# Performance work log

Measured on AMD Instinct MI355X. Metric: run time of the kernel, lower is better.

Reference implementation:

```python
import jax, jax.numpy as jnp
import numpy as np

D = 768
HID = 4 * D
B = 16
HRES = 32
WRES = 32
T = HRES * WRES


def layernorm(x, g, b, eps=1e-5):
    m = jnp.mean(x, axis=-1, keepdims=True)
    v = jnp.mean(jnp.square(x - m), axis=-1, keepdims=True)
    return (x - m) * jax.lax.rsqrt(v + eps) * g + b


def q_shift(x, H, W):
    # Vision-RWKV quad-directional token shift: split channels into 4 groups,
    # each group takes the neighboring patch's value in one direction (zero pad).
    Bn, N, C = x.shape
    xi = x.reshape(Bn, H, W, C)
    c = C // 4
    g0 = jnp.pad(xi[:, :, :-1, 0 * c:1 * c], ((0, 0), (0, 0), (1, 0), (0, 0)))  # from left
    g1 = jnp.pad(xi[:, :, 1:, 1 * c:2 * c], ((0, 0), (0, 0), (0, 1), (0, 0)))   # from right
    g2 = jnp.pad(xi[:, :-1, :, 2 * c:3 * c], ((0, 0), (1, 0), (0, 0), (0, 0)))  # from above
    g3 = jnp.pad(xi[:, 1:, :, 3 * c:4 * c], ((0, 0), (0, 1), (0, 0), (0, 0)))   # from below
    return jnp.concatenate([g0, g1, g2, g3], axis=-1).reshape(Bn, N, C)


def wkv_scan(w_log, u, k, v):
    # Numerically stable RWKV WKV recurrence (per-channel linear attention).
    # k, v: [B, T, C]; w = -exp(w_log) is the per-channel decay, u the bonus.
    w = -jnp.exp(w_log)
    kT = jnp.swapaxes(k, 0, 1)  # [T, B, C]
    vT = jnp.swapaxes(v, 0, 1)
    Bn, C = k.shape[0], k.shape[2]
    aa0 = jnp.zeros((Bn, C), k.dtype)
    bb0 = jnp.zeros((Bn, C), k.dtype)
    pp0 = jnp.full((Bn, C), -1e30, k.dtype)

    def step(carry, kv):
        aa, bb, pp = carry
        kt, vt = kv
        ww = u + kt
        p = jnp.maximum(pp, ww)
        e1 = jnp.exp(pp - p)
        e2 = jnp.exp(ww - p)
        out = (e1 * aa + e2 * vt) / (e1 * bb + e2)
        ww2 = pp + w
        p2 = jnp.maximum(ww2, kt)
        e1b = jnp.exp(ww2 - p2)
        e2b = jnp.exp(kt - p2)
        return (e1b * aa + e2b * vt, e1b * bb + e2b, p2), out

    _, outT = jax.lax.scan(step, (aa0, bb0, pp0), (kT, vT))
    return jnp.swapaxes(outT, 0, 1)  # [B, T, C]


def setup_inputs() -> dict:
    key = jax.random.key(0)
    ks = jax.random.split(key, 16)

    def nrm(k, shape, s=0.02):
        return jax.random.normal(k, shape, jnp.float32) * s

    return {
        "x": jax.random.normal(ks[0], (B, T, D), jnp.float32),
        "H": HRES,
        "W": WRES,
        "ln1_g": jnp.ones((D,), jnp.float32),
        "ln1_b": jnp.zeros((D,), jnp.float32),
        "ln2_g": jnp.ones((D,), jnp.float32),
        "ln2_b": jnp.zeros((D,), jnp.float32),
        "mu_k": jax.random.uniform(ks[1], (D,), jnp.float32),
        "mu_v": jax.random.uniform(ks[2], (D,), jnp.float32),
        "mu_r": jax.random.uniform(ks[3], (D,), jnp.float32),
        "w_log": nrm(ks[4], (D,), 0.5),
        "u": nrm(ks[5], (D,), 0.5),
        "Wk": nrm(ks[6], (D, D)),
        "Wv": nrm(ks[7], (D, D)),
        "Wr": nrm(ks[8], (D, D)),
        "Wo": nrm(ks[9], (D, D)),
        "cmu_k": jax.random.uniform(ks[10], (D,), jnp.float32),
        "cmu_r": jax.random.uniform(ks[11], (D,), jnp.float32),
        "Ck": nrm(ks[12], (HID, D)),
        "Cv": nrm(ks[13], (D, HID)),
        "Cr": nrm(ks[14], (D, D)),
    }


def reference(x, H, W, ln1_g, ln1_b, ln2_g, ln2_b, mu_k, mu_v, mu_r, w_log, u,
              Wk, Wv, Wr, Wo, cmu_k, cmu_r, Ck, Cv, Cr):
    h = x
    # ---- spatial mix (RWKV time-mix over patch sequence) ----
    a = layernorm(h, ln1_g, ln1_b)
    sx = q_shift(a, H, W)
    xk = a * mu_k + sx * (1.0 - mu_k)
    xv = a * mu_v + sx * (1.0 - mu_v)
    xr = a * mu_r + sx * (1.0 - mu_r)
    k = xk @ Wk.T
    v = xv @ Wv.T
    r = jax.nn.sigmoid(xr @ Wr.T)
    wkv = wkv_scan(w_log, u, k, v)
    h = h + (r * wkv) @ Wo.T
    # ---- channel mix (squared-ReLU gated FFN) ----
    a2 = layernorm(h, ln2_g, ln2_b)
    sx2 = q_shift(a2, H, W)
    xk2 = a2 * cmu_k + sx2 * (1.0 - cmu_k)
    xr2 = a2 * cmu_r + sx2 * (1.0 - cmu_r)
    kk = jnp.square(jax.nn.relu(xk2 @ Ck.T))
    h = h + jax.nn.sigmoid(xr2 @ Cr.T) * (kk @ Cv.T)
    # ---- outer residual from RWKVBlock.forward ----
    return h + x
```

## Files before the change

kernel.cpp:

```cpp
#include <hip/hip_runtime.h>
#include <hip/hip_bf16.h>

#define DD   768
#define TT   1024
#define BBATCH 16
#define NROWS (BBATCH * TT)
#define HIDN 3072
#define HHALF 1536
#define HH 32
#define WW 32
#define DW  (DD * DD)
#define DH  (DD * HIDN)
#define CCH 64
#define PCH (TT / CCH)

typedef float  floatx4 __attribute__((ext_vector_type(4)));
typedef __bf16 bf16x8  __attribute__((ext_vector_type(8)));

__device__ __forceinline__ float bf2f(__hip_bfloat16 v) { return __bfloat162float(v); }
__device__ __forceinline__ __hip_bfloat16 f2bf(float v) { return __float2bfloat16(v); }
__device__ __forceinline__ float toF(__hip_bfloat16 v) { return __bfloat162float(v); }
__device__ __forceinline__ float toF(float v) { return v; }

#define GL2LDS(gp, lp)  __builtin_amdgcn_global_load_lds(                     \
    (const __attribute__((address_space(1))) void*)(gp),                      \
    (__attribute__((address_space(3))) void*)(lp), 16, 0, 0)

__global__ __launch_bounds__(256)
void cvt_all(const float* __restrict__ w0, const float* __restrict__ w1,
             const float* __restrict__ w2, const float* __restrict__ w3,
             const float* __restrict__ w4, const float* __restrict__ w5,
             const float* __restrict__ w6, __hip_bfloat16* __restrict__ dst)
{
    const int b = blockIdx.x;
    const float* s; size_t dofs; int rel;
    if (b < 2880) {
        const int seg = b / 576; rel = b - seg * 576;
        s = seg == 0 ? w0 : seg == 1 ? w1 : seg == 2 ? w2 : seg == 3 ? w3 : w4;
        dofs = (size_t)seg * DW;
    } else if (b < 5184) {
        rel = b - 2880; s = w5; dofs = 5ull * DW;
    } else {
        rel = b - 5184; s = w6; dofs = 5ull * DW + DH;
    }
    const int i = rel * 1024 + threadIdx.x * 4;
    const float4 v = *reinterpret_cast<const float4*>(s + i);
    __hip_bfloat16 o[4] = {f2bf(v.x), f2bf(v.y), f2bf(v.z), f2bf(v.w)};
    *reinterpret_cast<ushort4*>(&dst[dofs + i]) = *reinterpret_cast<const ushort4*>(o);
}

template <typename TIN>
__global__ __launch_bounds__(256)
void ln_stats_k(const TIN* __restrict__ x,
                float* __restrict__ mean, float* __restrict__ rstd)
{
    const int row = blockIdx.x, tid = threadIdx.x;
    const int lane = tid & 63, wid = tid >> 6;
    const TIN* xr = x + (size_t)row * DD;
    float s1 = 0.f, s2 = 0.f;
#pragma unroll
    for (int i = 0; i < 3; ++i) {
        const float v = toF(xr[tid + i * 256]);
        s1 += v; s2 += v * v;
    }
#pragma unroll
    for (int off = 32; off > 0; off >>= 1) {
        s1 += __shfl_down(s1, off);
        s2 += __shfl_down(s2, off);
    }
    __shared__ float sh[8];
    if (lane == 0) { sh[wid] = s1; sh[4 + wid] = s2; }
    __syncthreads();
    if (tid == 0) {
        s1 = sh[0] + sh[1] + sh[2] + sh[3];
        s2 = sh[4] + sh[5] + sh[6] + sh[7];
        const float m = s1 * (1.f / DD);
        mean[row] = m;
        rstd[row] = rsqrtf(s2 * (1.f / DD) - m * m + 1e-5f);
    }
}

template <typename TIN>
__device__ __forceinline__ float ln_at(const TIN* __restrict__ x,
                                       const float* __restrict__ mean,
                                       const float* __restrict__ rstd,
                                       const float* __restrict__ g,
                                       const float* __restrict__ b,
                                       int grow, int c)
{
    return (toF(x[(size_t)grow * DD + c]) - mean[grow]) * rstd[grow] * g[c] + b[c];
}

template <typename TIN, int NOUT>
__global__ __launch_bounds__(256)
void mix_k(const TIN* __restrict__ x,
           const float* __restrict__ mean, const float* __restrict__ rstd,
           const float* __restrict__ g, const float* __restrict__ b,
           const float* __restrict__ muk,
           const float* __restrict__ muv,
           const float* __restrict__ mur,
           __hip_bfloat16* __restrict__ xk,
           __hip_bfloat16* __restrict__ xv,
           __hip_bfloat16* __restrict__ xr)
{
    const size_t idx = (size_t)blockIdx.x * 256 + threadIdx.x;
    const int c  = (int)(idx % DD);
    const int n  = (int)((idx / DD) % TT);
    const int bb = (int)(idx / ((size_t)DD * TT));
    const int y = n >> 5, xp = n & 31;
    const int grow = bb * TT + n;

    const float av = ln_at(x, mean, rstd, g, b, grow, c);

    const int grp = c / (DD / 4);
    int ny = y, nx = xp; bool ok;
    if      (grp == 0) { nx = xp - 1; ok = xp > 0;      }
    else if (grp == 1) { nx = xp + 1; ok = xp < WW - 1; }
    else if (grp == 2) { ny = y - 1;  ok = y > 0;       }
    else               { ny = y + 1;  ok = y < HH - 1;  }
    const float sx = ok ? ln_at(x, mean, rstd, g, b, bb * TT + ny * WW + nx, c) : 0.f;

    const float mk = muk[c], mr = mur[c];
    xk[idx] = f2bf(av * mk + sx * (1.f - mk));
    xr[idx] = f2bf(av * mr + sx * (1.f - mr));
    if (NOUT == 3) {
        const float mv = muv[c];
        xv[idx] = f2bf(av * mv + sx * (1.f - mv));
    }
}

#define BM 128
#define BN 128
#define BKK 64

__device__ __forceinline__ void gemm_core(
    const __hip_bfloat16* __restrict__ A, const __hip_bfloat16* __restrict__ W,
    int K, int Wstr, int bm, int bn, unsigned short* lds, floatx4 acc[4][4])
{
    const int tid  = threadIdx.x;
    const int lane = tid & 63, wid = tid >> 6;
    const int l15  = lane & 15, quad = lane >> 4;
    const int m0   = (wid & 1) * 64;
    const int n0   = (wid >> 1) * 64;
    const int srow  = lane >> 3;
    const int gcolg = (lane & 7) ^ srow;
    const int s0    = wid * 4;
    const int swzbase = l15 & 7;

    for (int k0 = 0; k0 < K; k0 += BKK) {
#pragma unroll
        for (int t = 0; t < 4; ++t) {
            const int s   = s0 + t;
            const int row = s * 8 + srow;
            GL2LDS(A + (size_t)(bm * BM + row) * K    + k0 + gcolg * 8,
                   &lds[s * 512]);
            GL2LDS(W + (size_t)(bn * BN + row) * Wstr + k0 + gcolg * 8,
                   &lds[8192 + s * 512]);
        }
        __syncthreads();
#pragma unroll
        for (int kk = 0; kk < BKK; kk += 32) {
            const int swz = (((kk >> 3) + quad) ^ swzbase) * 8;
            bf16x8 af[4], bfr[4];
#pragma unroll
            for (int i = 0; i < 4; ++i)
                af[i] = *reinterpret_cast<const bf16x8*>(
                    &lds[(m0 + i * 16 + l15) * BKK + swz]);
#pragma unroll
            for (int j = 0; j < 4; ++j)
                bfr[j] = *reinterpret_cast<const bf16x8*>(
                    &lds[8192 + (n0 + j * 16 + l15) * BKK + swz]);
#pragma unroll
            for (int i = 0; i < 4; ++i)
#pragma unroll
                for (int j = 0; j < 4; ++j)
                    acc[i][j] = __builtin_amdgcn_mfma_f32_16x16x32_bf16(
                        af[i], bfr[j], acc[i][j], 0, 0, 0);
        }
        __syncthreads();
    }
}

__device__ __forceinline__ void xpose_band(const floatx4 accRow[4], float* scr,
                                           int lane, float cv[16])
{
    const int l15 = lane & 15, quad = lane >> 4;
#pragma unroll
    for (int j = 0; j < 4; ++j)
#pragma unroll
        for (int r = 0; r < 4; ++r)
            scr[(quad * 4 + r) * 68 + j * 16 + l15] = accRow[j][r];
    const int row_l = lane >> 2, cb = (lane & 3) * 16;
#pragma unroll
    for (int q = 0; q < 4; ++q)
        *reinterpret_cast<float4*>(&cv[q * 4]) =
            *reinterpret_cast<const float4*>(&scr[row_l * 68 + cb + q * 4]);
}

template <int MODE>
__global__ __launch_bounds__(256, 2)
void gemm_bt(const __hip_bfloat16* __restrict__ A,
             const __hip_bfloat16* __restrict__ W,
             int K, int Wstr, int Nn,
             __hip_bfloat16* __restrict__ outB,
             float* __restrict__ outF,
             const __hip_bfloat16* __restrict__ auxS,
             const __hip_bfloat16* __restrict__ auxH,
             const float* __restrict__ auxX)
{
    __shared__ __align__(16) unsigned short lds[16384];
    const int bm = blockIdx.x, bn = blockIdx.y;
    const int tid = threadIdx.x, lane = tid & 63, wid = tid >> 6;
    const int m0 = (wid & 1) * 64, n0 = (wid >> 1) * 64;

    floatx4 acc[4][4];
#pragma unroll
    for (int i = 0; i < 4; ++i)
#pragma unroll
        for (int j = 0; j < 4; ++j)
            acc[i][j] = floatx4{0.f, 0.f, 0.f, 0.f};

    gemm_core(A, W, K, Wstr, bm, bn, lds, acc);

    float* scr = reinterpret_cast<float*>(lds) + wid * 1088;
    const int row_l = lane >> 2, cb = (lane & 3) * 16;
#pragma unroll
    for (int i = 0; i < 4; ++i) {
        float cv[16];
        xpose_band(acc[i], scr, lane, cv);
        const int grow = bm * BM + m0 + i * 16 + row_l;
        const int gcol = bn * BN + n0 + cb;
        const size_t idx = (size_t)grow * Nn + gcol;
        if (MODE == 1 || MODE == 3) {
            __hip_bfloat16 ob[16];
#pragma unroll
            for (int e = 0; e < 16; ++e) {
                float v = cv[e];
                if (MODE == 1) v = 1.f / (1.f + __expf(-v));
                else { v = fmaxf(v, 0.f); v = v * v; }
                ob[e] = f2bf(v);
            }
            *reinterpret_cast<uint4*>(&outB[idx])     = *reinterpret_cast<const uint4*>(&ob[0]);
            *reinterpret_cast<uint4*>(&outB[idx + 8]) = *reinterpret_cast<const uint4*>(&ob[8]);
        } else if (MODE == 2) {
            float xv[16];
#pragma unroll
            for (int q = 0; q < 4; ++q)
                *reinterpret_cast<float4*>(&xv[q * 4]) =
                    *reinterpret_cast<const float4*>(&auxX[idx + q * 4]);
            __hip_bfloat16 ob[16];
#pragma unroll
            for (int e = 0; e < 16; ++e) ob[e] = f2bf(cv[e] + xv[e]);
            *reinterpret_cast<uint4*>(&outB[idx])     = *reinterpret_cast<const uint4*>(&ob[0]);
            *reinterpret_cast<uint4*>(&outB[idx + 8]) = *reinterpret_cast<const uint4*>(&ob[8]);
        } else if (MODE == 4) {
            unsigned short hs[16], ss[16]; float xv[16], ov[16];
            *reinterpret_cast<uint4*>(&hs[0]) = *reinterpret_cast<const uint4*>(&auxH[idx]);
            *reinterpret_cast<uint4*>(&hs[8]) = *reinterpret_cast<const uint4*>(&auxH[idx + 8]);
            *reinterpret_cast<uint4*>(&ss[0]) = *reinterpret_cast<const uint4*>(&auxS[idx]);
            *reinterpret_cast<uint4*>(&ss[8]) = *reinterpret_cast<const uint4*>(&auxS[idx + 8]);
#pragma unroll
            for (int q = 0; q < 4; ++q)
                *reinterpret_cast<float4*>(&xv[q * 4]) =
                    *reinterpret_cast<const float4*>(&auxX[idx + q * 4]);
#pragma unroll
            for (int e = 0; e < 16; ++e)
                ov[e] = bf2f(__hip_bfloat16_raw{hs[e]})
                      + bf2f(__hip_bfloat16_raw{ss[e]}) * cv[e] + xv[e];
#pragma unroll
            for (int q = 0; q < 4; ++q)
                *reinterpret_cast<float4*>(&outF[idx + q * 4]) =
                    *reinterpret_cast<const float4*>(&ov[q * 4]);
        } else {
            unsigned short ss[16]; float ov[16];
            *reinterpret_cast<uint4*>(&ss[0]) = *reinterpret_cast<const uint4*>(&auxS[idx]);
            *reinterpret_cast<uint4*>(&ss[8]) = *reinterpret_cast<const uint4*>(&auxS[idx + 8]);
#pragma unroll
            for (int q = 0; q < 4; ++q)
                *reinterpret_cast<float4*>(&ov[q * 4]) =
                    *reinterpret_cast<const float4*>(&outF[idx + q * 4]);
#pragma unroll
            for (int e = 0; e < 16; ++e)
                ov[e] += bf2f(__hip_bfloat16_raw{ss[e]}) * cv[e];
#pragma unroll
            for (int q = 0; q < 4; ++q)
                *reinterpret_cast<float4*>(&outF[idx + q * 4]) =
                    *reinterpret_cast<const float4*>(&ov[q * 4]);
        }
    }
}

__global__ __launch_bounds__(256, 2)
void gemm_qkv(const __hip_bfloat16* __restrict__ A0, const __hip_bfloat16* __restrict__ A1,
              const __hip_bfloat16* __restrict__ A2,
              const __hip_bfloat16* __restrict__ W0, const __hip_bfloat16* __restrict__ W1,
              const __hip_bfloat16* __restrict__ W2,
              __hip_bfloat16* __restrict__ O0, __hip_bfloat16* __restrict__ O1,
              __hip_bfloat16* __restrict__ O2)
{
    __shared__ __align__(16) unsigned short lds[16384];
    const int z = blockIdx.z;
    const __hip_bfloat16* A = z == 0 ? A0 : z == 1 ? A1 : A2;
    const __hip_bfloat16* W = z == 0 ? W0 : z == 1 ? W1 : W2;
    __hip_bfloat16*       O = z == 0 ? O0 : z == 1 ? O1 : O2;
    const int bm = blockIdx.x, bn = blockIdx.y;
    const int tid = threadIdx.x, lane = tid & 63, wid = tid >> 6;
    const int m0 = (wid & 1) * 64, n0 = (wid >> 1) * 64;

    floatx4 acc[4][4];
#pragma unroll
    for (int i = 0; i < 4; ++i)
#pragma unroll
        for (int j = 0; j < 4; ++j)
            acc[i][j] = floatx4{0.f, 0.f, 0.f, 0.f};

    gemm_core(A, W, DD, DD, bm, bn, lds, acc);

    float* scr = reinterpret_cast<float*>(lds) + wid * 1088;
    const int row_l = lane >> 2, cb = (lane & 3) * 16;
#pragma unroll
    for (int i = 0; i < 4; ++i) {
        float cv[16];
        xpose_band(acc[i], scr, lane, cv);
        const int grow = bm * BM + m0 + i * 16 + row_l;
        const int gcol = bn * BN + n0 + cb;
        const size_t idx = (size_t)grow * DD + gcol;
        __hip_bfloat16 ob[16];
#pragma unroll
        for (int e = 0; e < 16; ++e) {
            float v = cv[e];
            if (z == 2) v = 1.f / (1.f + __expf(-v));
            ob[e] = f2bf(v);
        }
        *reinterpret_cast<uint4*>(&O[idx])     = *reinterpret_cast<const uint4*>(&ob[0]);
        *reinterpret_cast<uint4*>(&O[idx + 8]) = *reinterpret_cast<const uint4*>(&ob[8]);
    }
}

__global__ __launch_bounds__(256)
void wkv_passA(const float* __restrict__ w_log,
               const __hip_bfloat16* __restrict__ k,
               const __hip_bfloat16* __restrict__ v,
               float* __restrict__ SA, float* __restrict__ SB,
               float* __restrict__ SP)
{
    const int c  = blockIdx.x * 256 + threadIdx.x;
    const int j  = blockIdx.y;
    const int bb = blockIdx.z;
    const float w = -__expf(w_log[c]);
    const size_t base = ((size_t)bb * TT + j * CCH) * DD + c;
    float a = 0.f, b = 0.f, p = -1e30f;
#pragma unroll 4
    for (int t = 0; t < CCH; ++t) {
        const size_t o = base + (size_t)t * DD;
        const float kt = bf2f(k[o]);
        const float vt = bf2f(v[o]);
        const float ww2 = p + w;
        const float p2  = fmaxf(ww2, kt);
        const float e1  = __expf(ww2 - p2);
        const float e2  = __expf(kt - p2);
        a = e1 * a + e2 * vt;
        b = e1 * b + e2;
        p = p2;
    }
    const size_t si = ((size_t)bb * PCH + j) * DD + c;
    SA[si] = a; SB[si] = b; SP[si] = p;
}

__global__ __launch_bounds__(256)
void wkv_scanj(const float* __restrict__ w_log,
               float* __restrict__ SA, float* __restrict__ SB,
               float* __restrict__ SP)
{
    const int idx = blockIdx.x * 256 + threadIdx.x;
    const int c = idx % DD, bb = idx / DD;
    const float wC = -__expf(w_log[c]) * (float)CCH;
    float a = 0.f, b = 0.f, p = -1e30f;
#pragma unroll
    for (int j = 0; j < PCH; ++j) {
        const size_t si = ((size_t)bb * PCH + j) * DD + c;
        const float aj = SA[si], bj = SB[si], pj = SP[si];
        SA[si] = a; SB[si] = b; SP[si] = p;
        const float pd = p + wC;
        const float pn = fmaxf(pd, pj);
        const float e1 = __expf(pd - pn);
        const float e2 = __expf(pj - pn);
        a = e1 * a + e2 * aj;
        b = e1 * b + e2 * bj;
        p = pn;
    }
}

__global__ __launch_bounds__(256)
void wkv_passB(const float* __restrict__ w_log, const float* __restrict__ u,
               const __hip_bfloat16* __restrict__ k,
               const __hip_bfloat16* __restrict__ v,
               const __hip_bfloat16* __restrict__ r,
               __hip_bfloat16* __restrict__ rw,
               const float* __restrict__ SA, const float* __restrict__ SB,
               const float* __restrict__ SP)
{
    const int c  = blockIdx.x * 256 + threadIdx.x;
    const int j  = blockIdx.y;
    const int bb = blockIdx.z;
    const float w  = -__expf(w_log[c]);
    const float uu = u[c];
    const size_t si = ((size_t)bb * PCH + j) * DD + c;
    float aa = SA[si], bbv = SB[si], pp = SP[si];
    const size_t base = ((size_t)bb * TT + j * CCH) * DD + c;
#pragma unroll 4
    for (int t = 0; t < CCH; ++t) {
        const size_t o = base + (size_t)t * DD;
        const float kt = bf2f(k[o]);
        const float vt = bf2f(v[o]);
        const float rt = bf2f(r[o]);
        const float ww = uu + kt;
        const float p  = fmaxf(pp, ww);
        const float e1 = __expf(pp - p);
        const float e2 = __expf(ww - p);
        const float ov = __fdividef(e1 * aa + e2 * vt, e1 * bbv + e2);
        rw[o] = f2bf(rt * ov);
        const float ww2 = pp + w;
        const float p2  = fmaxf(ww2, kt);
        const float e1b = __expf(ww2 - p2);
        const float e2b = __expf(kt - p2);
        aa  = e1b * aa + e2b * vt;
        bbv = e1b * bbv + e2b;
        pp  = p2;
    }
}

extern "C" void kernel_launch(void* const* d_in, const int* in_sizes, int n_in,
                              void* d_out, int out_size, void* d_ws, size_t ws_size,
                              hipStream_t stream)
{
    (void)in_sizes; (void)n_in; (void)out_size;
    const float* x     = (const float*)d_in[0];
    const float* ln1_g = (const float*)d_in[3];
    const float* ln1_b = (const float*)d_in[4];
    const float* ln2_g = (const float*)d_in[5];
    const float* ln2_b = (const float*)d_in[6];
    const float* mu_k  = (const float*)d_in[7];
    const float* mu_v  = (const float*)d_in[8];
    const float* mu_r  = (const float*)d_in[9];
    const float* w_log = (const float*)d_in[10];
    const float* u     = (const float*)d_in[11];
    const float* Wk    = (const float*)d_in[12];
    const float* Wv    = (const float*)d_in[13];
    const float* Wr    = (const float*)d_in[14];
    const float* Wo    = (const float*)d_in[15];
    const float* cmu_k = (const float*)d_in[16];
    const float* cmu_r = (const float*)d_in[17];
    const float* Ck    = (const float*)d_in[18];
    const float* Cv    = (const float*)d_in[19];
    const float* Cr    = (const float*)d_in[20];
    float* out = (float*)d_out;

    const size_t ND = (size_t)NROWS * DD;
    const size_t SL = ND * 2;
    const size_t WBYTES = (size_t)(5 * DW + 2 * DH) * 2;
    const size_t NSTATE = (size_t)BBATCH * PCH * DD;
    const size_t NEED = 5 * SL + WBYTES
                      + 2 * (size_t)NROWS * sizeof(float)
                      + 3 * NSTATE * sizeof(float);
    if (ws_size < NEED) return;

    char* w = (char*)d_ws;
    __hip_bfloat16* S0 = (__hip_bfloat16*)(w);
    __hip_bfloat16* S1 = (__hip_bfloat16*)(w + 1 * SL);
    __hip_bfloat16* S2 = (__hip_bfloat16*)(w + 2 * SL);
    __hip_bfloat16* S3 = (__hip_bfloat16*)(w + 3 * SL);
    __hip_bfloat16* S4 = (__hip_bfloat16*)(w + 4 * SL);
    __hip_bfloat16* WB  = (__hip_bfloat16*)(w + 5 * SL);
    __hip_bfloat16* WkB = WB;
    __hip_bfloat16* WvB = WB + 1ull * DW;
    __hip_bfloat16* WrB = WB + 2ull * DW;
    __hip_bfloat16* WoB = WB + 3ull * DW;
    __hip_bfloat16* CrB = WB + 4ull * DW;
    __hip_bfloat16* CkB = WB + 5ull * DW;
    __hip_bfloat16* CvB = CkB + DH;
    float* meanB = (float*)(w + 5 * SL + WBYTES);
    float* rstdB = meanB + NROWS;
    float* SAb = rstdB + NROWS;
    float* SBb = SAb + NSTATE;
    float* SPb = SBb + NSTATE;

    const int EW_GRID = (int)(ND / 256);
    const dim3 g768(NROWS / BM, DD / BN);
    const dim3 g1536(NROWS / BM, HHALF / BN);
    const dim3 gqkv(NROWS / BM, DD / BN, 3);
    const dim3 gwkv(DD / 256, PCH, BBATCH);

    cvt_all<<<7488, 256, 0, stream>>>(Wk, Wv, Wr, Wo, Cr, Ck, Cv, WB);

    ln_stats_k<float><<<NROWS, 256, 0, stream>>>(x, meanB, rstdB);
    mix_k<float, 3><<<EW_GRID, 256, 0, stream>>>(x, meanB, rstdB, ln1_g, ln1_b,
                                                 mu_k, mu_v, mu_r, S0, S1, S2);
    gemm_qkv<<<dim3(NROWS / BM, DD / BN, 2), 256, 0, stream>>>(
        S0, S1, nullptr, WkB, WvB, nullptr, S3, S4, nullptr);
    gemm_bt<1><<<g768, 256, 0, stream>>>(S2, WrB, DD, DD, DD, S0, nullptr,
                                         nullptr, nullptr, nullptr);
    wkv_passA<<<gwkv, 256, 0, stream>>>(w_log, S3, S4, SAb, SBb, SPb);
    wkv_scanj<<<(BBATCH * DD) / 256, 256, 0, stream>>>(w_log, SAb, SBb, SPb);
    wkv_passB<<<gwkv, 256, 0, stream>>>(w_log, u, S3, S4, S0, S1, SAb, SBb, SPb);
    gemm_bt<2><<<g768, 256, 0, stream>>>(S1, WoB, DD, DD, DD, S2, nullptr,
                                         nullptr, nullptr, x);

    ln_stats_k<__hip_bfloat16><<<NROWS, 256, 0, stream>>>(S2, meanB, rstdB);
    mix_k<__hip_bfloat16, 2><<<EW_GRID, 256, 0, stream>>>(S2, meanB, rstdB, ln2_g, ln2_b,
                                                          cmu_k, nullptr, cmu_r, S0, nullptr, S3);
    gemm_bt<1><<<g768, 256, 0, stream>>>(S3, CrB, DD, DD, DD, S1, nullptr,
                                         nullptr, nullptr, nullptr);
    __hip_bfloat16* kk = S3;
    gemm_bt<3><<<g1536, 256, 0, stream>>>(S0, CkB, DD, DD, HHALF,
                                          kk, nullptr, nullptr, nullptr, nullptr);
    gemm_bt<4><<<g768, 256, 0, stream>>>(kk, CvB, HHALF, HIDN, DD,
                                         nullptr, out, S1, S2, x);
    gemm_bt<3><<<g1536, 256, 0, stream>>>(S0, CkB + (size_t)HHALF * DD, DD, DD, HHALF,
                                          kk, nullptr, nullptr, nullptr, nullptr);
    gemm_bt<5><<<g768, 256, 0, stream>>>(kk, CvB + HHALF, HHALF, HIDN, DD,
                                         nullptr, out, S1, nullptr, nullptr);
}
```

Before: 566.7 us.

## Vectorize LN/mix kernels and use extra workspace to fuse Wr and full-width FFN GEMMs

Vectorizes the layernorm statistics and token-shift mix kernels to four elements per thread, with one wave per row instead of a block-level reduction. When the workspace is large enough, it launches the receptance projection inside the batched QKV GEMM and runs the channel-mix Ck/Cv GEMMs at full hidden width instead of two halves. A six-slot variant writes the sigmoid gate to the output buffer and reads it back in a new epilogue. The aim is fewer launches, less partial-sum traffic and better memory coalescing, at the cost of more workspace and added code paths that depend on the workspace size.

```diff
diff --git a/kernel.cpp b/kernel.cpp
--- a/kernel.cpp
+++ b/kernel.cpp
@@ -22,6 +22,18 @@
 __device__ __forceinline__ float toF(__hip_bfloat16 v) { return __bfloat162float(v); }
 __device__ __forceinline__ float toF(float v) { return v; }
 
+__device__ __forceinline__ void load4f(const float* __restrict__ p, float o[4]) {
+    const float4 v = *reinterpret_cast<const float4*>(p);
+    o[0] = v.x; o[1] = v.y; o[2] = v.z; o[3] = v.w;
+}
+__device__ __forceinline__ void load4f(const __hip_bfloat16* __restrict__ p, float o[4]) {
+    const ushort4 v = *reinterpret_cast<const ushort4*>(p);
+    o[0] = bf2f(__hip_bfloat16_raw{v.x});
+    o[1] = bf2f(__hip_bfloat16_raw{v.y});
+    o[2] = bf2f(__hip_bfloat16_raw{v.z});
+    o[3] = bf2f(__hip_bfloat16_raw{v.w});
+}
+
 #define GL2LDS(gp, lp)  __builtin_amdgcn_global_load_lds(                     \
     (const __attribute__((address_space(1))) void*)(gp),                      \
     (__attribute__((address_space(3))) void*)(lp), 16, 0, 0)
@@ -54,41 +66,27 @@
 void ln_stats_k(const TIN* __restrict__ x,
                 float* __restrict__ mean, float* __restrict__ rstd)
 {
-    const int row = blockIdx.x, tid = threadIdx.x;
-    const int lane = tid & 63, wid = tid >> 6;
+    const int row  = blockIdx.x * 4 + (threadIdx.x >> 6);
+    const int lane = threadIdx.x & 63;
     const TIN* xr = x + (size_t)row * DD;
     float s1 = 0.f, s2 = 0.f;
 #pragma unroll
-    for (int i = 0; i < 3; ++i) {
-        const float v = toF(xr[tid + i * 256]);
-        s1 += v; s2 += v * v;
+    for (int q = 0; q < 3; ++q) {
+        float v4[4];
+        load4f(xr + 4 * lane + 256 * q, v4);
+#pragma unroll
+        for (int e = 0; e < 4; ++e) { s1 += v4[e]; s2 += v4[e] * v4[e]; }
     }
 #pragma unroll
     for (int off = 32; off > 0; off >>= 1) {
         s1 += __shfl_down(s1, off);
         s2 += __shfl_down(s2, off);
     }
-    __shared__ float sh[8];
-    if (lane == 0) { sh[wid] = s1; sh[4 + wid] = s2; }
-    __syncthreads();
-    if (tid == 0) {
-        s1 = sh[0] + sh[1] + sh[2] + sh[3];
-        s2 = sh[4] + sh[5] + sh[6] + sh[7];
+    if (lane == 0) {
         const float m = s1 * (1.f / DD);
         mean[row] = m;
         rstd[row] = rsqrtf(s2 * (1.f / DD) - m * m + 1e-5f);
     }
-}
-
-template <typename TIN>
-__device__ __forceinline__ float ln_at(const TIN* __restrict__ x,
-                                       const float* __restrict__ mean,
-                                       const float* __restrict__ rstd,
-                                       const float* __restrict__ g,
-                                       const float* __restrict__ b,
-                                       int grow, int c)
-{
-    return (toF(x[(size_t)grow * DD + c]) - mean[grow]) * rstd[grow] * g[c] + b[c];
 }
 
 template <typename TIN, int NOUT>
@@ -103,14 +101,12 @@
            __hip_bfloat16* __restrict__ xv,
            __hip_bfloat16* __restrict__ xr)
 {
-    const size_t idx = (size_t)blockIdx.x * 256 + threadIdx.x;
-    const int c  = (int)(idx % DD);
-    const int n  = (int)((idx / DD) % TT);
-    const int bb = (int)(idx / ((size_t)DD * TT));
+    const size_t i4 = ((size_t)blockIdx.x * 256 + threadIdx.x) * 4;
+    const int c  = (int)(i4 % DD);
+    const int n  = (int)((i4 / DD) % TT);
+    const int bb = (int)(i4 / ((size_t)DD * TT));
     const int y = n >> 5, xp = n & 31;
     const int grow = bb * TT + n;
-
-    const float av = ln_at(x, mean, rstd, g, b, grow, c);
 
     const int grp = c / (DD / 4);
     int ny = y, nx = xp; bool ok;
@@ -118,14 +114,48 @@
     else if (grp == 1) { nx = xp + 1; ok = xp < WW - 1; }
     else if (grp == 2) { ny = y - 1;  ok = y > 0;       }
     else               { ny = y + 1;  ok = y < HH - 1;  }
-    const float sx = ok ? ln_at(x, mean, rstd, g, b, bb * TT + ny * WW + nx, c) : 0.f;
-
-    const float mk = muk[c], mr = mur[c];
-    xk[idx] = f2bf(av * mk + sx * (1.f - mk));
-    xr[idx] = f2bf(av * mr + sx * (1.f - mr));
+
+    const float4 gv = *reinterpret_cast<const float4*>(g + c);
+    const float4 bv = *reinterpret_cast<const float4*>(b + c);
+    const float gg[4] = {gv.x, gv.y, gv.z, gv.w};
+    const float bbv[4] = {bv.x, bv.y, bv.z, bv.w};
+
+    float xc[4];
+    load4f(x + (size_t)grow * DD + c, xc);
+    const float m = mean[grow], rs = rstd[grow];
+    float av[4], sx[4] = {0.f, 0.f, 0.f, 0.f};
+#pragma unroll
+    for (int e = 0; e < 4; ++e) av[e] = (xc[e] - m) * rs * gg[e] + bbv[e];
+
+    if (ok) {
+        const int nrow = bb * TT + ny * WW + nx;
+        float xn[4];
+        load4f(x + (size_t)nrow * DD + c, xn);
+        const float m2 = mean[nrow], rs2 = rstd[nrow];
+#pragma unroll
+        for (int e = 0; e < 4; ++e) sx[e] = (xn[e] - m2) * rs2 * gg[e] + bbv[e];
+    }
+
+    const float4 mkv = *reinterpret_cast<const float4*>(muk + c);
+    const float4 mrv = *reinterpret_cast<const float4*>(mur + c);
+    const float mk[4] = {mkv.x, mkv.y, mkv.z, mkv.w};
+    const float mr[4] = {mrv.x, mrv.y, mrv.z, mrv.w};
+    __hip_bfloat16 ok4[4], or4[4];
+#pragma unroll
+    for (int e = 0; e < 4; ++e) {
+        ok4[e] = f2bf(av[e] * mk[e] + sx[e] * (1.f - mk[e]));
+        or4[e] = f2bf(av[e] * mr[e] + sx[e] * (1.f - mr[e]));
+    }
+    *reinterpret_cast<ushort4*>(&xk[i4]) = *reinterpret_cast<const ushort4*>(ok4);
+    *reinterpret_cast<ushort4*>(&xr[i4]) = *reinterpret_cast<const ushort4*>(or4);
     if (NOUT == 3) {
-        const float mv = muv[c];
-        xv[idx] = f2bf(av * mv + sx * (1.f - mv));
+        const float4 mvv = *reinterpret_cast<const float4*>(muv + c);
+        const float mv[4] = {mvv.x, mvv.y, mvv.z, mvv.w};
+        __hip_bfloat16 ov4[4];
+#pragma unroll
+        for (int e = 0; e < 4; ++e)
+            ov4[e] = f2bf(av[e] * mv[e] + sx[e] * (1.f - mv[e]));
+        *reinterpret_cast<ushort4*>(&xv[i4]) = *reinterpret_cast<const ushort4*>(ov4);
     }
 }
 
@@ -206,7 +236,8 @@
              float* __restrict__ outF,
              const __hip_bfloat16* __restrict__ auxS,
              const __hip_bfloat16* __restrict__ auxH,
-             const float* __restrict__ auxX)
+             const float* __restrict__ auxX,
+             const float* __restrict__ auxG)
 {
     __shared__ __align__(16) unsigned short lds[16384];
     const int bm = blockIdx.x, bn = blockIdx.y;
@@ -271,7 +302,7 @@
             for (int q = 0; q < 4; ++q)
                 *reinterpret_cast<float4*>(&outF[idx + q * 4]) =
                     *reinterpret_cast<const float4*>(&ov[q * 4]);
-        } else {
+        } else if (MODE == 5) {
             unsigned short ss[16]; float ov[16];
             *reinterpret_cast<uint4*>(&ss[0]) = *reinterpret_cast<const uint4*>(&auxS[idx]);
             *reinterpret_cast<uint4*>(&ss[8]) = *reinterpret_cast<const uint4*>(&auxS[idx + 8]);
@@ -282,6 +313,33 @@
 #pragma unroll
             for (int e = 0; e < 16; ++e)
                 ov[e] += bf2f(__hip_bfloat16_raw{ss[e]}) * cv[e];
+#pragma unroll
+            for (int q = 0; q < 4; ++q)
+                *reinterpret_cast<float4*>(&outF[idx + q * 4]) =
+                    *reinterpret_cast<const float4*>(&ov[q * 4]);
+        } else if (MODE == 6) {
+            unsigned short hs[16]; float xv[16], gf[16], ov[16];
+            *reinterpret_cast<uint4*>(&hs[0]) = *reinterpret_cast<const uint4*>(&auxH[idx]);
+            *reinterpret_cast<uint4*>(&hs[8]) = *reinterpret_cast<const uint4*>(&auxH[idx + 8]);
+#pragma unroll
+            for (int q = 0; q < 4; ++q) {
+                *reinterpret_cast<float4*>(&xv[q * 4]) =
+                    *reinterpret_cast<const float4*>(&auxX[idx + q * 4]);
+                *reinterpret_cast<float4*>(&gf[q * 4]) =
+                    *reinterpret_cast<const float4*>(&auxG[idx + q * 4]);
+            }
+#pragma unroll
+            for (int e = 0; e < 16; ++e)
+                ov[e] = bf2f(__hip_bfloat16_raw{hs[e]}) + gf[e] * cv[e] + xv[e];
+#pragma unroll
+            for (int q = 0; q < 4; ++q)
+                *reinterpret_cast<float4*>(&outF[idx + q * 4]) =
+                    *reinterpret_cast<const float4*>(&ov[q * 4]);
+        } else {
+            float ov[16];
+#pragma unroll
+            for (int e = 0; e < 16; ++e)
+                ov[e] = 1.f / (1.f + __expf(-cv[e]));
 #pragma unroll
             for (int q = 0; q < 4; ++q)
                 *reinterpret_cast<float4*>(&outF[idx + q * 4]) =
@@ -460,10 +518,13 @@
     const size_t SL = ND * 2;
     const size_t WBYTES = (size_t)(5 * DW + 2 * DH) * 2;
     const size_t NSTATE = (size_t)BBATCH * PCH * DD;
-    const size_t NEED = 5 * SL + WBYTES
-                      + 2 * (size_t)NROWS * sizeof(float)
+    const size_t TAIL = WBYTES + 2 * (size_t)NROWS * sizeof(float)
                       + 3 * NSTATE * sizeof(float);
-    if (ws_size < NEED) return;
+    int nslots;
+    if      (ws_size >= 7 * SL + TAIL) nslots = 7;
+    else if (ws_size >= 6 * SL + TAIL) nslots = 6;
+    else if (ws_size >= 5 * SL + TAIL) nslots = 5;
+    else return;
 
     char* w = (char*)d_ws;
     __hip_bfloat16* S0 = (__hip_bfloat16*)(w);
@@ -471,7 +532,8 @@
     __hip_bfloat16* S2 = (__hip_bfloat16*)(w + 2 * SL);
     __hip_bfloat16* S3 = (__hip_bfloat16*)(w + 3 * SL);
     __hip_bfloat16* S4 = (__hip_bfloat16*)(w + 4 * SL);
-    __hip_bfloat16* WB  = (__hip_bfloat16*)(w + 5 * SL);
+    __hip_bfloat16* S5 = (__hip_bfloat16*)(w + 5 * SL);
+    __hip_bfloat16* WB  = (__hip_bfloat16*)(w + (size_t)nslots * SL);
     __hip_bfloat16* WkB = WB;
     __hip_bfloat16* WvB = WB + 1ull * DW;
     __hip_bfloat16* WrB = WB + 2ull * DW;
@@ -479,45 +541,85 @@
     __hip_bfloat16* CrB = WB + 4ull * DW;
     __hip_bfloat16* CkB = WB + 5ull * DW;
     __hip_bfloat16* CvB = CkB + DH;
-    float* meanB = (float*)(w + 5 * SL + WBYTES);
+    float* meanB = (float*)(w + (size_t)nslots * SL + WBYTES);
     float* rstdB = meanB + NROWS;
     float* SAb = rstdB + NROWS;
     float* SBb = SAb + NSTATE;
     float* SPb = SBb + NSTATE;
 
-    const int EW_GRID = (int)(ND / 256);
+    const int LN_GRID  = NROWS / 4;
+    const int MIX_GRID = (int)(ND / 1024);
     const dim3 g768(NROWS / BM, DD / BN);
     const dim3 g1536(NROWS / BM, HHALF / BN);
-    const dim3 gqkv(NROWS / BM, DD / BN, 3);
+    const dim3 gCk(NROWS / BM, HIDN / BN);
+    const dim3 gqkv3(NROWS / BM, DD / BN, 3);
+    const dim3 gqkv2(NROWS / BM, DD / BN, 2);
     const dim3 gwkv(DD / 256, PCH, BBATCH);
 
     cvt_all<<<7488, 256, 0, stream>>>(Wk, Wv, Wr, Wo, Cr, Ck, Cv, WB);
 
-    ln_stats_k<float><<<NROWS, 256, 0, stream>>>(x, meanB, rstdB);
-    mix_k<float, 3><<<EW_GRID, 256, 0, stream>>>(x, meanB, rstdB, ln1_g, ln1_b,
-                                                 mu_k, mu_v, mu_r, S0, S1, S2);
-    gemm_qkv<<<dim3(NROWS / BM, DD / BN, 2), 256, 0, stream>>>(
-        S0, S1, nullptr, WkB, WvB, nullptr, S3, S4, nullptr);
-    gemm_bt<1><<<g768, 256, 0, stream>>>(S2, WrB, DD, DD, DD, S0, nullptr,
-                                         nullptr, nullptr, nullptr);
-    wkv_passA<<<gwkv, 256, 0, stream>>>(w_log, S3, S4, SAb, SBb, SPb);
-    wkv_scanj<<<(BBATCH * DD) / 256, 256, 0, stream>>>(w_log, SAb, SBb, SPb);
-    wkv_passB<<<gwkv, 256, 0, stream>>>(w_log, u, S3, S4, S0, S1, SAb, SBb, SPb);
-    gemm_bt<2><<<g768, 256, 0, stream>>>(S1, WoB, DD, DD, DD, S2, nullptr,
-                                         nullptr, nullptr, x);
-
-    ln_stats_k<__hip_bfloat16><<<NROWS, 256, 0, stream>>>(S2, meanB, rstdB);
-    mix_k<__hip_bfloat16, 2><<<EW_GRID, 256, 0, stream>>>(S2, meanB, rstdB, ln2_g, ln2_b,
-                                                          cmu_k, nullptr, cmu_r, S0, nullptr, S3);
-    gemm_bt<1><<<g768, 256, 0, stream>>>(S3, CrB, DD, DD, DD, S1, nullptr,
-                                         nullptr, nullptr, nullptr);
-    __hip_bfloat16* kk = S3;
-    gemm_bt<3><<<g1536, 256, 0, stream>>>(S0, CkB, DD, DD, HHALF,
-                                          kk, nullptr, nullptr, nullptr, nullptr);
-    gemm_bt<4><<<g768, 256, 0, stream>>>(kk, CvB, HHALF, HIDN, DD,
-                                         nullptr, out, S1, S2, x);
-    gemm_bt<3><<<g1536, 256, 0, stream>>>(S0, CkB + (size_t)HHALF * DD, DD, DD, HHALF,
-                                          kk, nullptr, nullptr, nullptr, nullptr);
-    gemm_bt<5><<<g768, 256, 0, stream>>>(kk, CvB + HHALF, HHALF, HIDN, DD,
-                                         nullptr, out, S1, nullptr, nullptr);
-}
+    ln_stats_k<float><<<LN_GRID, 256, 0, stream>>>(x, meanB, rstdB);
+    mix_k<float, 3><<<MIX_GRID, 256, 0, stream>>>(x, meanB, rstdB, ln1_g, ln1_b,
+                                                  mu_k, mu_v, mu_r, S0, S1, S2);
+
+    if (nslots == 7) {
+        gemm_qkv<<<gqkv3, 256, 0, stream>>>(S0, S1, S2, WkB, WvB, WrB, S3, S4, S5);
+        wkv_passA<<<gwkv, 256, 0, stream>>>(w_log, S3, S4, SAb, SBb, SPb);
+        wkv_scanj<<<(BBATCH * DD) / 256, 256, 0, stream>>>(w_log, SAb, SBb, SPb);
+        wkv_passB<<<gwkv, 256, 0, stream>>>(w_log, u, S3, S4, S5, S1, SAb, SBb, SPb);
+        gemm_bt<2><<<g768, 256, 0, stream>>>(S1, WoB, DD, DD, DD, S2, nullptr,
+                                             nullptr, nullptr, x, nullptr);
+        ln_stats_k<__hip_bfloat16><<<LN_GRID, 256, 0, stream>>>(S2, meanB, rstdB);
+        mix_k<__hip_bfloat16, 2><<<MIX_GRID, 256, 0, stream>>>(S2, meanB, rstdB, ln2_g, ln2_b,
+                                                               cmu_k, nullptr, cmu_r,
+                                                               S0, nullptr, S3);
+        gemm_bt<1><<<g768, 256, 0, stream>>>(S3, CrB, DD, DD, DD, S1, nullptr,
+                                             nullptr, nullptr, nullptr, nullptr);
+        gemm_bt<3><<<gCk, 256, 0, stream>>>(S0, CkB, DD, DD, HIDN,
+                                            S3, nullptr, nullptr, nullptr, nullptr, nullptr);
+        gemm_bt<4><<<g768, 256, 0, stream>>>(S3, CvB, HIDN, HIDN, DD,
+                                             nullptr, out, S1, S2, x, nullptr);
+    } else if (nslots == 6) {
+        gemm_qkv<<<gqkv3, 256, 0, stream>>>(S0, S1, S2, WkB, WvB, WrB, S3, S4, S5);
+        wkv_passA<<<gwkv, 256, 0, stream>>>(w_log, S3, S4, SAb, SBb, SPb);
+        wkv_scanj<<<(BBATCH * DD) / 256, 256, 0, stream>>>(w_log, SAb, SBb, SPb);
+        wkv_passB<<<gwkv, 256, 0, stream>>>(w_log, u, S3, S4, S5, S0, SAb, SBb, SPb);
+        gemm_bt<2><<<g768, 256, 0, stream>>>(S0, WoB, DD, DD, DD, S1, nullptr,
+                                             nullptr, nullptr, x, nullptr);
+        ln_stats_k<__hip_bfloat16><<<LN_GRID, 256, 0, stream>>>(S1, meanB, rstdB);
+        mix_k<__hip_bfloat16, 2><<<MIX_GRID, 256, 0, stream>>>(S1, meanB, rstdB, ln2_g, ln2_b,
+                                                               cmu_k, nullptr, cmu_r,
+                                                               S0, nullptr, S2);
+        gemm_bt<7><<<g768, 256, 0, stream>>>(S2, CrB, DD, DD, DD, nullptr, out,
+                                             nullptr, nullptr, nullptr, nullptr);
+        gemm_bt<3><<<gCk, 256, 0, stream>>>(S0, CkB, DD, DD, HIDN,
+                                            S2, nullptr, nullptr, nullptr, nullptr, nullptr);
+        gemm_bt<6><<<g768, 256, 0, stream>>>(S2, CvB, HIDN, HIDN, DD,
+                                             nullptr, out, nullptr, S1, x, out);
+    } else {
+        gemm_qkv<<<gqkv2, 256, 0, stream>>>(S0, S1, nullptr, WkB, WvB, nullptr,
+                                            S3, S4, nullptr);
+        gemm_bt<1><<<g768, 256, 0, stream>>>(S2, WrB, DD, DD, DD, S0, nullptr,
+                                             nullptr, nullptr, nullptr, nullptr);
+        wkv_passA<<<gwkv, 256, 0, stream>>>(w_log, S3, S4, SAb, SBb, SPb);
+        wkv_scanj<<<(BBATCH * DD) / 256, 256, 0, stream>>>(w_log, SAb, SBb, SPb);
+        wkv_passB<<<gwkv, 256, 0, stream>>>(w_log, u, S3, S4, S0, S1, SAb, SBb, SPb);
+        gemm_bt<2><<<g768, 256, 0, stream>>>(S1, WoB, DD, DD, DD, S2, nullptr,
+                                             nullptr, nullptr, x, nullptr);
+        ln_stats_k<__hip_bfloat16><<<LN_GRID, 256, 0, stream>>>(S2, meanB, rstdB);
+        mix_k<__hip_bfloat16, 2><<<MIX_GRID, 256, 0, stream>>>(S2, meanB, rstdB, ln2_g, ln2_b,
+                                                               cmu_k, nullptr, cmu_r,
+                                                               S0, nullptr, S3);
+        gemm_bt<1><<<g768, 256, 0, stream>>>(S3, CrB, DD, DD, DD, S1, nullptr,
+                                             nullptr, nullptr, nullptr, nullptr);
+        __hip_bfloat16* kk = S3;
+        gemm_bt<3><<<g1536, 256, 0, stream>>>(S0, CkB, DD, DD, HHALF,
+                                              kk, nullptr, nullptr, nullptr, nullptr, nullptr);
+        gemm_bt<4><<<g768, 256, 0, stream>>>(kk, CvB, HHALF, HIDN, DD,
+                                             nullptr, out, S1, S2, x, nullptr);
+        gemm_bt<3><<<g1536, 256, 0, stream>>>(S0, CkB + (size_t)HHALF * DD, DD, DD, HHALF,
+                                              kk, nullptr, nullptr, nullptr, nullptr, nullptr);
+        gemm_bt<5><<<g768, 256, 0, stream>>>(kk, CvB + HHALF, HHALF, HIDN, DD,
+                                             nullptr, out, S1, nullptr, nullptr, nullptr);
+    }
+}
```

Result: faster. 534.4 us (-5.7%).
